# Kernel optimization log

Hardware: AMD Instinct MI355X
Metric: run time of the kernel (lower is better)

The kernel has to match this reference:

```python
import jax, jax.numpy as jnp
import numpy as np

CHANNELS = 1024
N_HEADS = 16
N_EMBD = 512
H_DIM = CHANNELS // N_HEADS


def setup_inputs() -> dict:
    key = jax.random.key(0)
    ks = jax.random.split(key, 10)
    b, hw = 16, 4096
    s = 0.02
    return {
        "x": jax.random.normal(ks[0], (b, hw, CHANNELS), dtype=jnp.float32),
        "p": jax.random.normal(ks[1], (b, 77, N_EMBD), dtype=jnp.float32),
        "Wq": jax.random.normal(ks[2], (CHANNELS, CHANNELS), dtype=jnp.float32) * s,
        "bq": jnp.zeros((CHANNELS,), dtype=jnp.float32),
        "Wk": jax.random.normal(ks[3], (N_EMBD, CHANNELS), dtype=jnp.float32) * s,
        "bk": jnp.zeros((CHANNELS,), dtype=jnp.float32),
        "Wv": jax.random.normal(ks[4], (N_EMBD, CHANNELS), dtype=jnp.float32) * s,
        "bv": jnp.zeros((CHANNELS,), dtype=jnp.float32),
        "Ww": jax.random.normal(ks[5], (CHANNELS, CHANNELS), dtype=jnp.float32) * s,
        "bw": jnp.zeros((CHANNELS,), dtype=jnp.float32),
    }


def reference(x, p, Wq, bq, Wk, bk, Wv, bv, Ww, bw):
    b, hw, c = x.shape
    # Linear projections (torch Linear: y = x @ W^T + b; here weights stored as (in, out))
    q = x @ Wq + bq                      # (b, hw, c)
    k = p @ Wk + bk                      # (b, 77, c)
    v = p @ Wv + bv                      # (b, 77, c)
    q = q.reshape(b, hw, N_HEADS, H_DIM)
    k = k.reshape(b, 77, N_HEADS, H_DIM)
    v = v.reshape(b, 77, N_HEADS, H_DIM)
    scale = 1.0 / jnp.sqrt(jnp.asarray(H_DIM, dtype=x.dtype))
    # scores: (b, heads, hw, 77)
    scores = jnp.einsum("bqhd,bkhd->bhqk", q, k) * scale
    attn = jax.nn.softmax(scores, axis=-1)
    out = jnp.einsum("bhqk,bkhd->bqhd", attn, v).reshape(b, hw, c)
    return out @ Ww + bw
```

## Files before the change

kernel.cpp:

```cpp
#include <hip/hip_runtime.h>
#include <cstdint>
#include <type_traits>

typedef uint16_t u16;
typedef uint32_t u32;
typedef __attribute__((ext_vector_type(4))) float f32x4;
typedef __attribute__((ext_vector_type(8))) __bf16 vbf8;
typedef __attribute__((ext_vector_type(8))) short vs8;

template <typename T, typename = void>
struct CanMfma : std::false_type {};
template <typename T>
struct CanMfma<T, std::void_t<decltype(__builtin_amdgcn_mfma_f32_16x16x32_bf16(
    std::declval<T>(), std::declval<T>(), std::declval<f32x4>(), 0, 0, 0))>>
    : std::true_type {};
typedef std::conditional_t<CanMfma<vbf8>::value, vbf8, vs8> frag_t;

__device__ __forceinline__ f32x4 mfma_bf16(frag_t a, frag_t b, f32x4 c) {
  return __builtin_amdgcn_mfma_f32_16x16x32_bf16(a, b, c, 0, 0, 0);
}

__device__ __forceinline__ u16 f2bf(float f) {
  u32 u = __builtin_bit_cast(u32, f);
  u32 r = (u + 0x7FFFu + ((u >> 16) & 1u)) >> 16;
  return (u16)r;
}

__device__ __forceinline__ void gload_lds16(const void* g, void* l) {
  __builtin_amdgcn_global_load_lds(
      (const __attribute__((address_space(1))) void*)g,
      (__attribute__((address_space(3))) void*)l, 16, 0, 0);
}

__global__ __launch_bounds__(256) void cast_f32_bf16(
    const float* __restrict__ in, u16* __restrict__ out, int n8) {
  int i = blockIdx.x * 256 + threadIdx.x;
  const int stride = gridDim.x * 256;
  for (; i < n8; i += stride) {
    const float4 a  = ((const float4*)in)[(size_t)i * 2];
    const float4 b2 = ((const float4*)in)[(size_t)i * 2 + 1];
    uint4 o;
    o.x = (u32)f2bf(a.x)  | ((u32)f2bf(a.y)  << 16);
    o.y = (u32)f2bf(a.z)  | ((u32)f2bf(a.w)  << 16);
    o.z = (u32)f2bf(b2.x) | ((u32)f2bf(b2.y) << 16);
    o.w = (u32)f2bf(b2.z) | ((u32)f2bf(b2.w) << 16);
    ((uint4*)out)[(size_t)i] = o;
  }
}

__global__ __launch_bounds__(256) void transpose_cast(
    const float* __restrict__ in, u16* __restrict__ out, int K, int N) {
  __shared__ float tile[32][33];
  const int k0 = blockIdx.x * 32, n0 = blockIdx.y * 32;
  const int tr = threadIdx.x >> 5, tc = threadIdx.x & 31;
#pragma unroll
  for (int i = 0; i < 4; ++i)
    tile[tr + i * 8][tc] = in[(size_t)(k0 + tr + i * 8) * N + (n0 + tc)];
  __syncthreads();
#pragma unroll
  for (int i = 0; i < 4; ++i)
    out[(size_t)(n0 + tr + i * 8) * K + (k0 + tc)] = f2bf(tile[tc][tr + i * 8]);
}

template <bool OUT_BF16>
__global__ __launch_bounds__(256) void gemm_bt(
    const u16* __restrict__ A, const u16* __restrict__ Bt,
    const float* __restrict__ bias, void* __restrict__ Cout,
    int M, int N, int K, int Mtiles, int Ntiles) {
  __shared__ char Al[2][128 * 32 * 2];
  __shared__ char Bl[2][128 * 32 * 2];

  const int nwg = Mtiles * Ntiles;
  int bid = (int)blockIdx.x;
  bid = (bid & 7) * (nwg >> 3) + (bid >> 3);
  const int mt = bid / Ntiles, nt = bid % Ntiles;
  const int m0 = mt * 128, n0 = nt * 128;

  const int tid = (int)threadIdx.x;
  const int lane = tid & 63;
  const int wv = tid >> 6;
  const int wm = wv & 1, wn = wv >> 1;
  const int lr = lane & 15, lg = lane >> 4;
  const int rsub = lane >> 2;
  const int slot = lane & 3;
  const int rb0 = n0 + rsub;

  auto stage = [&](int buf, int t) {
    const int k0 = t << 5;
#pragma unroll
    for (int c = 0; c < 2; ++c) {
      const int ci = c * 4 + wv;
      int rra = m0 + ci * 16 + rsub;
      if (rra >= M) rra = M - 1;
      gload_lds16(A + (size_t)rra * K + k0 + slot * 8, Al[buf] + ci * 1024);
      const int rrb = rb0 + ci * 16;
      gload_lds16(Bt + (size_t)rrb * K + k0 + slot * 8, Bl[buf] + ci * 1024);
    }
  };

  f32x4 zero4 = {0.f, 0.f, 0.f, 0.f};
  f32x4 acc[4][4];
#pragma unroll
  for (int i = 0; i < 4; ++i)
#pragma unroll
    for (int j = 0; j < 4; ++j) acc[i][j] = zero4;

  const int nk = K >> 5;
  int cur = 0;
  stage(0, 0);
  __syncthreads();

  for (int t = 0; t < nk; ++t) {
    if (t + 1 < nk) stage(cur ^ 1, t + 1);
    frag_t af[4], bf[4];
#pragma unroll
    for (int i = 0; i < 4; ++i) {
      af[i] = *(const frag_t*)(Al[cur] + (wm * 64 + i * 16 + lr) * 64 + lg * 16);
      bf[i] = *(const frag_t*)(Bl[cur] + (wn * 64 + i * 16 + lr) * 64 + lg * 16);
    }
#pragma unroll
    for (int i = 0; i < 4; ++i)
#pragma unroll
      for (int j = 0; j < 4; ++j)
        acc[i][j] = mfma_bf16(af[i], bf[j], acc[i][j]);
    __syncthreads();
    cur ^= 1;
  }

#pragma unroll
  for (int j = 0; j < 4; ++j) {
    const int col = n0 + wn * 64 + j * 16 + lr;
    const float bv = bias[col];
#pragma unroll
    for (int i = 0; i < 4; ++i) {
      const int rbase = m0 + wm * 64 + i * 16 + lg * 4;
#pragma unroll
      for (int r = 0; r < 4; ++r) {
        const int row = rbase + r;
        const float val = acc[i][j][r] + bv;
        if constexpr (OUT_BF16) {
          u32 me = f2bf(val);
          u32 other = __shfl_xor(me, 1);
          if ((lane & 1) == 0 && row < M) {
            *(u32*)((u16*)Cout + (size_t)row * N + col) = me | (other << 16);
          }
        } else {
          if (row < M) ((float*)Cout)[(size_t)row * N + col] = val;
        }
      }
    }
  }
}

template <bool OUT_BF16>
__global__ __launch_bounds__(512, 4) void gemm256(
    const u16* __restrict__ A, const u16* __restrict__ Bt,
    const float* __restrict__ bias, void* __restrict__ Cout,
    int M, int N, int K) {
  __shared__ u16 Al[2][256 * 32];
  __shared__ u16 Bl[2][128 * 32];

  const int Ntiles = N >> 7;
  const int nwg = (M >> 8) * Ntiles;
  int bid = (int)blockIdx.x;
  bid = (bid & 7) * (nwg >> 3) + (bid >> 3);
  const int mt = bid / Ntiles, ntl = bid % Ntiles;
  const int m0 = mt << 8, n0 = ntl << 7;

  const int tid = (int)threadIdx.x;
  const int lane = tid & 63;
  const int wid = tid >> 6;
  const int wm = wid >> 1, wn = wid & 1;
  const int lr = lane & 15, lg = lane >> 4;

  const int srow = lane >> 2;
  const int sslot = (lane & 3) ^ ((lane >> 3) & 3);
  const u16* Abase = A + (size_t)(m0 + wid * 32 + srow) * K + sslot * 8;
  const u16* Bbase = Bt + (size_t)(n0 + wid * 16 + srow) * K + sslot * 8;

  auto stage = [&](u16* da, u16* db, int t) {
    const int k0 = t << 5;
    gload_lds16(Abase + k0, (char*)da + wid * 2048);
    gload_lds16(Abase + ((size_t)K << 4) + k0, (char*)da + wid * 2048 + 1024);
    gload_lds16(Bbase + k0, (char*)db + wid * 1024);
  };

  auto ldsF = [&](const u16* base, int row) -> frag_t {
    const int phys = lg ^ ((row >> 1) & 3);
    return *(const frag_t*)(base + (size_t)row * 32 + phys * 8);
  };

  f32x4 zero4 = {0.f, 0.f, 0.f, 0.f};
  f32x4 acc[4][4];
#pragma unroll
  for (int i = 0; i < 4; ++i)
#pragma unroll
    for (int j = 0; j < 4; ++j) acc[i][j] = zero4;

  const int nt = K >> 5;
  const int ar0 = wm * 64 + lr;
  const int br0 = wn * 64 + lr;

  stage(&Al[0][0], &Bl[0][0], 0);
  stage(&Al[1][0], &Bl[1][0], 1);
  asm volatile("s_waitcnt vmcnt(3)" ::: "memory");
  __builtin_amdgcn_s_barrier();

  for (int t = 0; t < nt; ++t) {
    const int cur = t & 1;
    const u16* al = &Al[cur][0];
    const u16* bl = &Bl[cur][0];
    if (t >= 1 && t + 1 < nt)
      stage(&Al[cur ^ 1][0], &Bl[cur ^ 1][0], t + 1);
    frag_t a[4], b[4];
#pragma unroll
    for (int i = 0; i < 4; ++i) a[i] = ldsF(al, ar0 + i * 16);
#pragma unroll
    for (int j = 0; j < 4; ++j) b[j] = ldsF(bl, br0 + j * 16);
#pragma unroll
    for (int i = 0; i < 4; ++i)
#pragma unroll
      for (int j = 0; j < 4; ++j)
        acc[i][j] = mfma_bf16(a[i], b[j], acc[i][j]);
    if (t + 1 < nt) {
      asm volatile("s_waitcnt vmcnt(0)" ::: "memory");
      __builtin_amdgcn_s_barrier();
    }
  }

  float bvv[4];
#pragma unroll
  for (int bj = 0; bj < 4; ++bj) bvv[bj] = bias[n0 + wn * 64 + bj * 16 + lr];
#pragma unroll
  for (int ai = 0; ai < 4; ++ai) {
    const int rbase = m0 + wm * 64 + ai * 16 + lg * 4;
#pragma unroll
    for (int rr = 0; rr < 4; ++rr) {
      const int row = rbase + rr;
#pragma unroll
      for (int bj = 0; bj < 4; ++bj) {
        const int cb = n0 + wn * 64 + bj * 16;
        const float val = acc[ai][bj][rr] + bvv[bj];
        if constexpr (OUT_BF16) {
          u32 me = f2bf(val);
          u32 d0 = me | (__shfl_xor(me, 1) << 16);
          u32 d1 = __shfl_xor(d0, 2);
          if ((lane & 3) == 0) {
            uint2 o; o.x = d0; o.y = d1;
            *(uint2*)((u16*)Cout + (size_t)row * N + cb + (lr & 12)) = o;
          }
        } else {
          float v0 = val;
          float v1 = __shfl_xor(v0, 1);
          float v2 = __shfl_xor(v0, 2);
          float v3 = __shfl_xor(v1, 2);
          if ((lane & 3) == 0) {
            float4 o; o.x = v0; o.y = v1; o.z = v2; o.w = v3;
            *(float4*)((float*)Cout + (size_t)row * N + cb + (lr & 12)) = o;
          }
        }
      }
    }
  }
}

__global__ __launch_bounds__(256) void attn_kernel(
    const u16* __restrict__ Q, const u16* __restrict__ K,
    const u16* __restrict__ V, u16* __restrict__ O) {
  __shared__ u16 Kl[96][72];
  __shared__ u16 Vt[64][104];

  const int bid = blockIdx.x;
  const int qt = bid & 63;
  const int h = (bid >> 6) & 15;
  const int b = bid >> 10;
  const int tid = threadIdx.x;

#pragma unroll
  for (int it = 0; it < 3; ++it) {
    const int idx = tid + it * 256;
    const int key = idx >> 3, s = idx & 7;
    uint4 val{0u, 0u, 0u, 0u};
    if (key < 77)
      val = *(const uint4*)(K + ((size_t)(b * 77 + key)) * 1024 + h * 64 + s * 8);
    *(uint4*)(&Kl[key][s * 8]) = val;
  }
#pragma unroll
  for (int it = 0; it < 3; ++it) {
    const int idx = tid + it * 256;
    if (idx < 616) {
      const int key = idx >> 3, s = idx & 7;
      const uint4 v4 =
          *(const uint4*)(V + ((size_t)(b * 77 + key)) * 1024 + h * 64 + s * 8);
      const u16* e = (const u16*)&v4;
#pragma unroll
      for (int j = 0; j < 8; ++j) Vt[s * 8 + j][key] = e[j];
    }
  }
#pragma unroll
  for (int it = 0; it < 5; ++it) {
    const int idx = tid + it * 256;
    if (idx < 1216) {
      const int d = idx / 19, kk = 77 + idx % 19;
      Vt[d][kk] = 0;
    }
  }
  __syncthreads();

  const int lane = tid & 63;
  const int wv = tid >> 6;
  const int lr = lane & 15;
  const int lg = lane >> 4;

  const size_t qrow = (size_t)(b * 4096 + qt * 64 + wv * 16 + lr) * 1024 + h * 64;
  frag_t qf[2];
#pragma unroll
  for (int ks = 0; ks < 2; ++ks)
    qf[ks] = *(const frag_t*)(Q + qrow + ks * 32 + lg * 8);

  f32x4 zero4 = {0.f, 0.f, 0.f, 0.f};
  f32x4 sa[5] = {zero4, zero4, zero4, zero4, zero4};
#pragma unroll
  for (int ks = 0; ks < 2; ++ks) {
#pragma unroll
    for (int kt = 0; kt < 5; ++kt) {
      frag_t kf = *(const frag_t*)(&Kl[kt * 16 + lr][ks * 32 + lg * 8]);
      sa[kt] = mfma_bf16(kf, qf[ks], sa[kt]);
    }
  }

  float p[5][4];
  float mx = -3.0e38f;
#pragma unroll
  for (int kt = 0; kt < 5; ++kt)
#pragma unroll
    for (int r = 0; r < 4; ++r) {
      const int key = kt * 16 + lg * 4 + r;
      float s = sa[kt][r] * 0.125f;
      if (key >= 77) s = -3.0e38f;
      p[kt][r] = s;
      mx = fmaxf(mx, s);
    }
  mx = fmaxf(mx, __shfl_xor(mx, 16));
  mx = fmaxf(mx, __shfl_xor(mx, 32));
  float sum = 0.f;
#pragma unroll
  for (int kt = 0; kt < 5; ++kt)
#pragma unroll
    for (int r = 0; r < 4; ++r) {
      const float e = __expf(p[kt][r] - mx);
      p[kt][r] = e;
      sum += e;
    }
  sum += __shfl_xor(sum, 16);
  sum += __shfl_xor(sum, 32);
  const float rden = 1.0f / sum;
#pragma unroll
  for (int kt = 0; kt < 5; ++kt)
#pragma unroll
    for (int r = 0; r < 4; ++r) p[kt][r] *= rden;

  union FP { frag_t v; u16 e[8]; };
  frag_t pa[3];
#pragma unroll
  for (int kb = 0; kb < 3; ++kb) {
    FP f;
#pragma unroll
    for (int j = 0; j < 8; ++j) {
      const int kt = 2 * kb + (j >> 2);
      f.e[j] = (kt < 5) ? f2bf(p[kt][j & 3]) : (u16)0;
    }
    pa[kb] = f.v;
  }

  f32x4 oa[4] = {zero4, zero4, zero4, zero4};
#pragma unroll
  for (int nt = 0; nt < 4; ++nt) {
    const int d = nt * 16 + lr;
#pragma unroll
    for (int kb = 0; kb < 3; ++kb) {
      const int key0 = kb * 32 + lg * 4;
      FP vb;
      *(uint2*)(&vb.e[0]) = *(const uint2*)(&Vt[d][key0]);
      *(uint2*)(&vb.e[4]) = *(const uint2*)(&Vt[d][key0 + 16]);
      oa[nt] = mfma_bf16(pa[kb], vb.v, oa[nt]);
    }
  }

#pragma unroll
  for (int nt = 0; nt < 4; ++nt)
#pragma unroll
    for (int r = 0; r < 4; ++r) {
      const int qr = wv * 16 + lg * 4 + r;
      u32 me = f2bf(oa[nt][r]);
      u32 other = __shfl_xor(me, 1);
      if ((lane & 1) == 0) {
        *(u32*)(O + ((size_t)(b * 4096 + qt * 64 + qr)) * 1024 + h * 64 +
                nt * 16 + lr) = me | (other << 16);
      }
    }
}

extern "C" void kernel_launch(void* const* d_in, const int* in_sizes, int n_in,
                              void* d_out, int out_size, void* d_ws, size_t ws_size,
                              hipStream_t stream) {
  const float* x  = (const float*)d_in[0];
  const float* p  = (const float*)d_in[1];
  const float* Wq = (const float*)d_in[2];
  const float* bq = (const float*)d_in[3];
  const float* Wk = (const float*)d_in[4];
  const float* bk = (const float*)d_in[5];
  const float* Wv = (const float*)d_in[6];
  const float* bv = (const float*)d_in[7];
  const float* Ww = (const float*)d_in[8];
  const float* bw = (const float*)d_in[9];

  char* ws = (char*)d_ws;
  if (ws_size < 281034752ULL) return;

  u16* x_bf = (u16*)(ws + 0);
  u16* q_bf = (u16*)(ws + 134217728);
  u16* wq_t = (u16*)(ws + 268435456);
  u16* ww_t = (u16*)(ws + 270532608);
  u16* wk_t = (u16*)(ws + 272629760);
  u16* wv_t = (u16*)(ws + 273678336);
  u16* p_bf = (u16*)(ws + 274726912);
  u16* k_bf = (u16*)(ws + 275988480);
  u16* v_bf = (u16*)(ws + 278511616);

  cast_f32_bf16<<<4096, 256, 0, stream>>>(x, x_bf, 8388608);
  cast_f32_bf16<<<308, 256, 0, stream>>>(p, p_bf, 78848);
  transpose_cast<<<dim3(32, 32), 256, 0, stream>>>(Wq, wq_t, 1024, 1024);
  transpose_cast<<<dim3(32, 32), 256, 0, stream>>>(Ww, ww_t, 1024, 1024);
  transpose_cast<<<dim3(16, 32), 256, 0, stream>>>(Wk, wk_t, 512, 1024);
  transpose_cast<<<dim3(16, 32), 256, 0, stream>>>(Wv, wv_t, 512, 1024);

  gemm_bt<true><<<80, 256, 0, stream>>>(p_bf, wk_t, bk, k_bf, 1232, 1024, 512, 10, 8);
  gemm_bt<true><<<80, 256, 0, stream>>>(p_bf, wv_t, bv, v_bf, 1232, 1024, 512, 10, 8);
  gemm256<true><<<2048, 512, 0, stream>>>(x_bf, wq_t, bq, q_bf, 65536, 1024, 1024);
  attn_kernel<<<16384, 256, 0, stream>>>(q_bf, k_bf, v_bf, x_bf);
  gemm256<false><<<2048, 512, 0, stream>>>(x_bf, ww_t, bw, d_out, 65536, 1024, 1024);
}
```

Measured before the change: 633.9 us.

## Fuse fp32-to-bf16 cast of x into the Q projection GEMM

Removes the separate cast kernel that converted the whole x tensor to bf16. The Q GEMM now stages fp32 tiles of x into LDS with a new swizzle and converts to bf16 when building MFMA fragments. This saves a full write and re-read of a bf16 copy of x. In exchange, the GEMM reads twice the A bytes from global memory and doubles A's LDS footprint, which may lower occupancy. The conversion is also repeated by each wave that reads a given A row.

```diff
diff --git a/kernel.cpp b/kernel.cpp
--- a/kernel.cpp
+++ b/kernel.cpp
@@ -24,6 +24,25 @@
   u32 u = __builtin_bit_cast(u32, f);
   u32 r = (u + 0x7FFFu + ((u >> 16) & 1u)) >> 16;
   return (u16)r;
+}
+
+template <typename FT = frag_t>
+__device__ __forceinline__ FT cvt8_bf16(float4 lo, float4 hi) {
+  if constexpr (std::is_same<FT, vbf8>::value) {
+    vbf8 f;
+    f[0] = (__bf16)lo.x; f[1] = (__bf16)lo.y;
+    f[2] = (__bf16)lo.z; f[3] = (__bf16)lo.w;
+    f[4] = (__bf16)hi.x; f[5] = (__bf16)hi.y;
+    f[6] = (__bf16)hi.z; f[7] = (__bf16)hi.w;
+    return f;
+  } else {
+    union { FT v; u16 e[8]; } f;
+    f.e[0] = f2bf(lo.x); f.e[1] = f2bf(lo.y);
+    f.e[2] = f2bf(lo.z); f.e[3] = f2bf(lo.w);
+    f.e[4] = f2bf(hi.x); f.e[5] = f2bf(hi.y);
+    f.e[6] = f2bf(hi.z); f.e[7] = f2bf(hi.w);
+    return f.v;
+  }
 }
 
 __device__ __forceinline__ void gload_lds16(const void* g, void* l) {
@@ -152,13 +171,17 @@
   }
 }
 
-template <bool OUT_BF16>
+template <bool OUT_BF16, bool A_F32>
 __global__ __launch_bounds__(512, 4) void gemm256(
-    const u16* __restrict__ A, const u16* __restrict__ Bt,
+    const void* __restrict__ Ain, const u16* __restrict__ Bt,
     const float* __restrict__ bias, void* __restrict__ Cout,
     int M, int N, int K) {
-  __shared__ u16 Al[2][256 * 32];
+  constexpr int AHALF = A_F32 ? 16384 : 8192;
+  __shared__ u16 Al[2][AHALF];
   __shared__ u16 Bl[2][128 * 32];
+
+  const u16* A16 = (const u16*)Ain;
+  const float* A32 = (const float*)Ain;
 
   const int Ntiles = N >> 7;
   const int nwg = (M >> 8) * Ntiles;
@@ -173,22 +196,50 @@
   const int wm = wid >> 1, wn = wid & 1;
   const int lr = lane & 15, lg = lane >> 4;
 
-  const int srow = lane >> 2;
-  const int sslot = (lane & 3) ^ ((lane >> 3) & 3);
-  const u16* Abase = A + (size_t)(m0 + wid * 32 + srow) * K + sslot * 8;
-  const u16* Bbase = Bt + (size_t)(n0 + wid * 16 + srow) * K + sslot * 8;
+  const u16* Bbase = Bt + (size_t)(n0 + wid * 16 + (lane >> 2)) * K +
+                     ((lane & 3) ^ ((lane >> 3) & 3)) * 8;
+  const u16* Abase16 =
+      A_F32 ? nullptr
+            : A16 + (size_t)(m0 + wid * 32 + (lane >> 2)) * K +
+                  ((lane & 3) ^ ((lane >> 3) & 3)) * 8;
+  const float* Abase32 =
+      A_F32 ? A32 + (size_t)(m0 + wid * 32 + (lane >> 3)) * K +
+                  ((lane & 7) ^ (lane >> 3)) * 4
+            : nullptr;
 
   auto stage = [&](u16* da, u16* db, int t) {
     const int k0 = t << 5;
-    gload_lds16(Abase + k0, (char*)da + wid * 2048);
-    gload_lds16(Abase + ((size_t)K << 4) + k0, (char*)da + wid * 2048 + 1024);
+    if constexpr (A_F32) {
+      const float* g = Abase32 + k0;
+      char* l = (char*)da + wid * 4096;
+      gload_lds16(g, l);
+      gload_lds16(g + ((size_t)K << 3), l + 1024);
+      gload_lds16(g + ((size_t)K << 4), l + 2048);
+      gload_lds16(g + (size_t)K * 24, l + 3072);
+    } else {
+      gload_lds16(Abase16 + k0, (char*)da + wid * 2048);
+      gload_lds16(Abase16 + ((size_t)K << 4) + k0, (char*)da + wid * 2048 + 1024);
+    }
     gload_lds16(Bbase + k0, (char*)db + wid * 1024);
   };
 
-  auto ldsF = [&](const u16* base, int row) -> frag_t {
+  auto ldsB = [&](const u16* base, int row) -> frag_t {
     const int phys = lg ^ ((row >> 1) & 3);
     return *(const frag_t*)(base + (size_t)row * 32 + phys * 8);
   };
+  auto ldsA = [&](const u16* base, int row) -> frag_t {
+    if constexpr (A_F32) {
+      const float* bp = (const float*)base;
+      const int s0 = (2 * lg) ^ (row & 7);
+      const int s1 = (2 * lg + 1) ^ (row & 7);
+      float4 lo = *(const float4*)(bp + (size_t)row * 32 + s0 * 4);
+      float4 hi = *(const float4*)(bp + (size_t)row * 32 + s1 * 4);
+      return cvt8_bf16(lo, hi);
+    } else {
+      const int phys = lg ^ ((row >> 1) & 3);
+      return *(const frag_t*)(base + (size_t)row * 32 + phys * 8);
+    }
+  };
 
   f32x4 zero4 = {0.f, 0.f, 0.f, 0.f};
   f32x4 acc[4][4];
@@ -203,7 +254,10 @@
 
   stage(&Al[0][0], &Bl[0][0], 0);
   stage(&Al[1][0], &Bl[1][0], 1);
-  asm volatile("s_waitcnt vmcnt(3)" ::: "memory");
+  if constexpr (A_F32)
+    asm volatile("s_waitcnt vmcnt(5)" ::: "memory");
+  else
+    asm volatile("s_waitcnt vmcnt(3)" ::: "memory");
   __builtin_amdgcn_s_barrier();
 
   for (int t = 0; t < nt; ++t) {
@@ -214,9 +268,9 @@
       stage(&Al[cur ^ 1][0], &Bl[cur ^ 1][0], t + 1);
     frag_t a[4], b[4];
 #pragma unroll
-    for (int i = 0; i < 4; ++i) a[i] = ldsF(al, ar0 + i * 16);
-#pragma unroll
-    for (int j = 0; j < 4; ++j) b[j] = ldsF(bl, br0 + j * 16);
+    for (int i = 0; i < 4; ++i) a[i] = ldsA(al, ar0 + i * 16);
+#pragma unroll
+    for (int j = 0; j < 4; ++j) b[j] = ldsB(bl, br0 + j * 16);
 #pragma unroll
     for (int i = 0; i < 4; ++i)
 #pragma unroll
@@ -418,7 +472,7 @@
   char* ws = (char*)d_ws;
   if (ws_size < 281034752ULL) return;
 
-  u16* x_bf = (u16*)(ws + 0);
+  u16* ao_bf = (u16*)(ws + 0);
   u16* q_bf = (u16*)(ws + 134217728);
   u16* wq_t = (u16*)(ws + 268435456);
   u16* ww_t = (u16*)(ws + 270532608);
@@ -428,7 +482,6 @@
   u16* k_bf = (u16*)(ws + 275988480);
   u16* v_bf = (u16*)(ws + 278511616);
 
-  cast_f32_bf16<<<4096, 256, 0, stream>>>(x, x_bf, 8388608);
   cast_f32_bf16<<<308, 256, 0, stream>>>(p, p_bf, 78848);
   transpose_cast<<<dim3(32, 32), 256, 0, stream>>>(Wq, wq_t, 1024, 1024);
   transpose_cast<<<dim3(32, 32), 256, 0, stream>>>(Ww, ww_t, 1024, 1024);
@@ -437,7 +490,8 @@
 
   gemm_bt<true><<<80, 256, 0, stream>>>(p_bf, wk_t, bk, k_bf, 1232, 1024, 512, 10, 8);
   gemm_bt<true><<<80, 256, 0, stream>>>(p_bf, wv_t, bv, v_bf, 1232, 1024, 512, 10, 8);
-  gemm256<true><<<2048, 512, 0, stream>>>(x_bf, wq_t, bq, q_bf, 65536, 1024, 1024);
-  attn_kernel<<<16384, 256, 0, stream>>>(q_bf, k_bf, v_bf, x_bf);
-  gemm256<false><<<2048, 512, 0, stream>>>(x_bf, ww_t, bw, d_out, 65536, 1024, 1024);
-}
+  gemm256<true, true><<<2048, 512, 0, stream>>>(x, wq_t, bq, q_bf, 65536, 1024, 1024);
+  attn_kernel<<<16384, 256, 0, stream>>>(q_bf, k_bf, v_bf, ao_bf);
+  gemm256<false, false><<<2048, 512, 0, stream>>>(ao_bf, ww_t, bw, d_out,
+                                                  65536, 1024, 1024);
+}
```

Measured after the change: 636.5 us. About the same (+0.4%).

## Rewrite big GEMM with triple-buffered K=64 tiles and interleaved quarter-MFMA pipeline

Applied to the files above, without the earlier changes.

The main 256x128 GEMM now uses K-tiles of 64 with three LDS buffers, so global loads run two tiles ahead. The inner loop is split into four MFMA quadrants, with LDS fragment loads and async global staging interleaved between them and barriers placed to overlap memory with compute. The shared-memory swizzle is changed to an 8-slot XOR and MFMA sections get raised wave priority. LDS use grows to about 144KB per block, so launch bounds drop to 2 blocks per CU, trading occupancy for deeper pipelining.

```diff
diff --git a/kernel.cpp b/kernel.cpp
--- a/kernel.cpp
+++ b/kernel.cpp
@@ -153,12 +153,12 @@
 }
 
 template <bool OUT_BF16>
-__global__ __launch_bounds__(512, 4) void gemm256(
+__global__ __launch_bounds__(512, 2) void gemm_p4(
     const u16* __restrict__ A, const u16* __restrict__ Bt,
     const float* __restrict__ bias, void* __restrict__ Cout,
     int M, int N, int K) {
-  __shared__ u16 Al[2][256 * 32];
-  __shared__ u16 Bl[2][128 * 32];
+  __shared__ u16 Al[3][256 * 64];
+  __shared__ u16 Bl[3][128 * 64];
 
   const int Ntiles = N >> 7;
   const int nwg = (M >> 8) * Ntiles;
@@ -173,21 +173,27 @@
   const int wm = wid >> 1, wn = wid & 1;
   const int lr = lane & 15, lg = lane >> 4;
 
-  const int srow = lane >> 2;
-  const int sslot = (lane & 3) ^ ((lane >> 3) & 3);
-  const u16* Abase = A + (size_t)(m0 + wid * 32 + srow) * K + sslot * 8;
-  const u16* Bbase = Bt + (size_t)(n0 + wid * 16 + srow) * K + sslot * 8;
-
-  auto stage = [&](u16* da, u16* db, int t) {
-    const int k0 = t << 5;
-    gload_lds16(Abase + k0, (char*)da + wid * 2048);
-    gload_lds16(Abase + ((size_t)K << 4) + k0, (char*)da + wid * 2048 + 1024);
-    gload_lds16(Bbase + k0, (char*)db + wid * 1024);
+  const int sslot = (lane & 7) ^ (lane >> 3);
+  const u16* Ab = A + (size_t)(m0 + wid * 16 + (lane >> 3)) * K + sslot * 8;
+  const u16* Bb = Bt + (size_t)(n0 + wid * 16 + (lane >> 3)) * K + sslot * 8;
+  const int ldsWOff = wid * 16 * 64;
+
+  auto stageAH = [&](int buf, int H, int t) {
+    const u16* g = Ab + (size_t)H * 128 * K + t * 64;
+    u16* l = &Al[buf][H * 8192 + ldsWOff];
+    gload_lds16(g, l);
+    gload_lds16(g + (size_t)8 * K, l + 512);
   };
-
-  auto ldsF = [&](const u16* base, int row) -> frag_t {
-    const int phys = lg ^ ((row >> 1) & 3);
-    return *(const frag_t*)(base + (size_t)row * 32 + phys * 8);
+  auto stageB = [&](int buf, int t) {
+    const u16* g = Bb + t * 64;
+    u16* l = &Bl[buf][ldsWOff];
+    gload_lds16(g, l);
+    gload_lds16(g + (size_t)8 * K, l + 512);
+  };
+
+  auto ldsF = [&](const u16* base, int row, int ks) -> frag_t {
+    const int phys = ((ks << 2) + lg) ^ (row & 7);
+    return *(const frag_t*)(base + (size_t)row * 64 + phys * 8);
   };
 
   f32x4 zero4 = {0.f, 0.f, 0.f, 0.f};
@@ -197,35 +203,81 @@
 #pragma unroll
     for (int j = 0; j < 4; ++j) acc[i][j] = zero4;
 
-  const int nt = K >> 5;
-  const int ar0 = wm * 64 + lr;
-  const int br0 = wn * 64 + lr;
-
-  stage(&Al[0][0], &Bl[0][0], 0);
-  stage(&Al[1][0], &Bl[1][0], 1);
-  asm volatile("s_waitcnt vmcnt(3)" ::: "memory");
+  frag_t a[2][2], b0[2][2], b1[2][2];
+
+  auto mmq = [&](frag_t (&bb)[2][2], int ro, int co) {
+    __builtin_amdgcn_s_setprio(1);
+#pragma unroll
+    for (int i = 0; i < 2; ++i)
+#pragma unroll
+      for (int j = 0; j < 2; ++j) {
+        acc[ro + i][co + j] = mfma_bf16(a[i][0], bb[j][0], acc[ro + i][co + j]);
+        acc[ro + i][co + j] = mfma_bf16(a[i][1], bb[j][1], acc[ro + i][co + j]);
+      }
+    __builtin_amdgcn_s_setprio(0);
+  };
+
+  const int nt = K >> 6;
+
+  stageAH(0, 0, 0); stageAH(0, 1, 0); stageB(0, 0);
+  stageAH(1, 0, 1); stageAH(1, 1, 1); stageB(1, 1);
+  asm volatile("s_waitcnt vmcnt(6)" ::: "memory");
   __builtin_amdgcn_s_barrier();
 
+  int c = 0;
   for (int t = 0; t < nt; ++t) {
-    const int cur = t & 1;
-    const u16* al = &Al[cur][0];
-    const u16* bl = &Bl[cur][0];
-    if (t >= 1 && t + 1 < nt)
-      stage(&Al[cur ^ 1][0], &Bl[cur ^ 1][0], t + 1);
-    frag_t a[4], b[4];
-#pragma unroll
-    for (int i = 0; i < 4; ++i) a[i] = ldsF(al, ar0 + i * 16);
-#pragma unroll
-    for (int j = 0; j < 4; ++j) b[j] = ldsF(bl, br0 + j * 16);
-#pragma unroll
-    for (int i = 0; i < 4; ++i)
-#pragma unroll
-      for (int j = 0; j < 4; ++j)
-        acc[i][j] = mfma_bf16(a[i], b[j], acc[i][j]);
-    if (t + 1 < nt) {
+    const u16* bufA = &Al[c][0];
+    const u16* bufB = &Bl[c][0];
+    const int c2 = (c + 2 >= 3) ? c - 1 : c + 2;
+    const bool st = (t + 2) < nt;
+#pragma unroll
+    for (int i = 0; i < 2; ++i) {
+      a[i][0] = ldsF(bufA, wm * 64 + i * 16 + lr, 0);
+      a[i][1] = ldsF(bufA, wm * 64 + i * 16 + lr, 1);
+    }
+#pragma unroll
+    for (int j = 0; j < 2; ++j) {
+      b0[j][0] = ldsF(bufB, wn * 64 + j * 16 + lr, 0);
+      b0[j][1] = ldsF(bufB, wn * 64 + j * 16 + lr, 1);
+    }
+    if (st) stageAH(c2, 0, t + 2);
+    __builtin_amdgcn_sched_barrier(0);
+    __builtin_amdgcn_s_barrier();
+    asm volatile("s_waitcnt lgkmcnt(0)" ::: "memory");
+    __builtin_amdgcn_sched_barrier(0);
+    mmq(b0, 0, 0);
+    __builtin_amdgcn_s_barrier();
+#pragma unroll
+    for (int j = 0; j < 2; ++j) {
+      b1[j][0] = ldsF(bufB, wn * 64 + 32 + j * 16 + lr, 0);
+      b1[j][1] = ldsF(bufB, wn * 64 + 32 + j * 16 + lr, 1);
+    }
+    if (st) stageAH(c2, 1, t + 2);
+    __builtin_amdgcn_sched_barrier(0);
+    __builtin_amdgcn_s_barrier();
+    asm volatile("s_waitcnt lgkmcnt(0)" ::: "memory");
+    __builtin_amdgcn_sched_barrier(0);
+    mmq(b1, 0, 2);
+    __builtin_amdgcn_s_barrier();
+#pragma unroll
+    for (int i = 0; i < 2; ++i) {
+      a[i][0] = ldsF(bufA, wm * 64 + 32 + i * 16 + lr, 0);
+      a[i][1] = ldsF(bufA, wm * 64 + 32 + i * 16 + lr, 1);
+    }
+    if (st) stageB(c2, t + 2);
+    __builtin_amdgcn_sched_barrier(0);
+    __builtin_amdgcn_s_barrier();
+    asm volatile("s_waitcnt lgkmcnt(0)" ::: "memory");
+    __builtin_amdgcn_sched_barrier(0);
+    mmq(b1, 2, 2);
+    __builtin_amdgcn_s_barrier();
+    mmq(b0, 2, 0);
+    if (st)
+      asm volatile("s_waitcnt vmcnt(6)" ::: "memory");
+    else if (t + 2 == nt)
       asm volatile("s_waitcnt vmcnt(0)" ::: "memory");
-      __builtin_amdgcn_s_barrier();
-    }
+    if (t + 1 < nt) __builtin_amdgcn_s_barrier();
+    c = (c + 1 >= 3) ? 0 : c + 1;
   }
 
   float bvv[4];
@@ -437,7 +489,7 @@
 
   gemm_bt<true><<<80, 256, 0, stream>>>(p_bf, wk_t, bk, k_bf, 1232, 1024, 512, 10, 8);
   gemm_bt<true><<<80, 256, 0, stream>>>(p_bf, wv_t, bv, v_bf, 1232, 1024, 512, 10, 8);
-  gemm256<true><<<2048, 512, 0, stream>>>(x_bf, wq_t, bq, q_bf, 65536, 1024, 1024);
+  gemm_p4<true><<<2048, 512, 0, stream>>>(x_bf, wq_t, bq, q_bf, 65536, 1024, 1024);
   attn_kernel<<<16384, 256, 0, stream>>>(q_bf, k_bf, v_bf, x_bf);
-  gemm256<false><<<2048, 512, 0, stream>>>(x_bf, ww_t, bw, d_out, 65536, 1024, 1024);
-}
+  gemm_p4<false><<<2048, 512, 0, stream>>>(x_bf, ww_t, bw, d_out, 65536, 1024, 1024);
+}
```

After: 804.1 us. 26.9% more time.
